# Kernel optimization log

Measured on AMD Instinct MI355X. Metric: run time of the kernel, lower is better.

Reference implementation:

```python
import jax, jax.numpy as jnp
import numpy as np

N = 100000   # nodes
E = 1600000  # edges
D = 128      # feature dim (layers all 128)
G = 512      # graphs in batch
C = 10       # num_classes
EPS = 1e-5   # batchnorm eps


def setup_inputs() -> dict:
    key = jax.random.key(0)
    ks = jax.random.split(key, 16)
    s = 1.0 / np.sqrt(D)
    return {
        "x": jax.random.normal(ks[0], (N, D), jnp.float32),
        "edge_index": jax.random.randint(ks[1], (2, E), 0, N),
        "batch": jnp.sort(jax.random.randint(ks[2], (N,), 0, G)),
        "w1": jax.random.normal(ks[3], (D, D), jnp.float32) * s,
        "b1": jnp.zeros((D,), jnp.float32),
        "w2": jax.random.normal(ks[4], (D, D), jnp.float32) * s,
        "b2": jnp.zeros((D,), jnp.float32),
        "w3": jax.random.normal(ks[5], (D, D), jnp.float32) * s,
        "b3": jnp.zeros((D,), jnp.float32),
        "g1": jnp.ones((D,), jnp.float32),
        "be1": jnp.zeros((D,), jnp.float32),
        "g2": jnp.ones((D,), jnp.float32),
        "be2": jnp.zeros((D,), jnp.float32),
        "fc_w": jax.random.normal(ks[6], (D, C), jnp.float32) * s,
        "fc_b": jnp.zeros((C,), jnp.float32),
    }


def _gcn(x, src, dst, norm, W, b):
    # transform -> gather -> normalize -> scatter-add (PyG GCNConv)
    h = x @ W
    out = jax.ops.segment_sum(h[src] * norm[:, None], dst, num_segments=x.shape[0])
    return out + b


def _bn(x, g, b):
    # training-mode BatchNorm1d: batch mean / biased variance
    mu = jnp.mean(x, axis=0)
    var = jnp.mean((x - mu) ** 2, axis=0)
    return (x - mu) * jax.lax.rsqrt(var + EPS) * g + b


def reference(x, edge_index, batch, w1, b1, w2, b2, w3, b3, g1, be1, g2, be2, fc_w, fc_b):
    n = x.shape[0]
    loop = jnp.arange(n)
    src = jnp.concatenate([edge_index[0], loop])  # add self-loops
    dst = jnp.concatenate([edge_index[1], loop])
    deg = jax.ops.segment_sum(jnp.ones_like(src, x.dtype), dst, num_segments=n)
    dinv = jax.lax.rsqrt(jnp.maximum(deg, 1.0))  # deg >= 1 due to self-loops
    norm = dinv[src] * dinv[dst]  # symmetric normalization per edge

    h = jax.nn.relu(_gcn(x, src, dst, norm, w1, b1))        # conv1 + relu (bn1 unused, per source)
    h = jax.nn.relu(_gcn(h, src, dst, norm, w2, b2))        # conv2 + relu
    h = jax.nn.relu(_bn(h, g1, be1))                        # bn + relu
    h = jax.nn.relu(_gcn(h, src, dst, norm, w3, b3))        # conv3 + relu
    h = jax.nn.relu(_bn(h, g2, be2))                        # bn + relu

    cnt = jax.ops.segment_sum(jnp.ones((n,), h.dtype), batch, num_segments=G)
    pooled = jax.ops.segment_sum(h, batch, num_segments=G) / jnp.maximum(cnt, 1.0)[:, None]
    logits = pooled @ fc_w + fc_b
    return jax.nn.log_softmax(logits, axis=1)
```

## Files before the change

### kernel.cpp

```cpp
#include <hip/hip_runtime.h>
#include <hip/hip_bf16.h>
#include <math.h>

#define D 128
#define G_GRAPHS 512
#define C_CLASSES 10
#define BN_EPS 1e-5f
#define NBUCK_MAX 512
#define EDGE_CHUNK 4096
#define EPT 16

typedef unsigned short u16;
typedef unsigned int u32;
typedef unsigned short ushort4_t __attribute__((ext_vector_type(4)));
typedef unsigned short ushort8_t __attribute__((ext_vector_type(8)));
typedef __bf16 bf16x8 __attribute__((ext_vector_type(8)));
typedef float floatx4 __attribute__((ext_vector_type(4)));
union B8 { ushort8_t u; bf16x8 b; };

__device__ __forceinline__ float bf_lo(u32 v) { return __uint_as_float(v << 16); }
__device__ __forceinline__ float bf_hi(u32 v) { return __uint_as_float(v & 0xffff0000u); }
__device__ __forceinline__ u16 f2bf(float f) {
    union { float f; u32 u; } x; x.f = f;
    u32 r = x.u + 0x7fff + ((x.u >> 16) & 1);
    return (u16)(r >> 16);
}
__device__ __forceinline__ u32 pack2bf(float a, float b) {
    return (u32)f2bf(a) | ((u32)f2bf(b) << 16);
}


__global__ __launch_bounds__(256) void bucket_hist_kernel(
    const int* __restrict__ dst, int* __restrict__ bucketCnt, int E, int nbuck)
{
    __shared__ int h[NBUCK_MAX];
    int tid = threadIdx.x;
    for (int i = tid; i < NBUCK_MAX; i += 256) h[i] = 0;
    __syncthreads();
    for (int i = blockIdx.x * 256 + tid; i < E; i += gridDim.x * 256)
        atomicAdd(&h[dst[i] >> 8], 1);
    __syncthreads();
    for (int i = tid; i < nbuck; i += 256)
        if (h[i]) atomicAdd(&bucketCnt[i], h[i]);
}

__global__ void scan_buckets_kernel(
    const int* __restrict__ bucketCnt, int* __restrict__ bucketBase,
    int* __restrict__ bucketCursor, int* __restrict__ rowPtr, int nbuck, int N, int E)
{
    __shared__ int buf[2][512];
    int tid = threadIdx.x;
    int v = (tid < nbuck) ? bucketCnt[tid] : 0;
    buf[0][tid] = v;
    __syncthreads();
    int cur = 0;
    for (int off = 1; off < 512; off <<= 1) {
        buf[1 - cur][tid] = buf[cur][tid] + ((tid >= off) ? buf[cur][tid - off] : 0);
        cur ^= 1;
        __syncthreads();
    }
    if (tid < nbuck) {
        int b = buf[cur][tid] - v;
        bucketBase[tid] = b;
        bucketCursor[tid] = b;
    }
    if (tid == 0) { bucketBase[nbuck] = E; rowPtr[N] = E; }
}

__global__ __launch_bounds__(256) void scatter_pairs_kernel(
    const int* __restrict__ src, const int* __restrict__ dst,
    int* __restrict__ bucketCursor, u32* __restrict__ pairs, int E)
{
    __shared__ int h[NBUCK_MAX];
    __shared__ int base[NBUCK_MAX];
    int tid = threadIdx.x;
    int e0 = blockIdx.x * EDGE_CHUNK;
    for (int i = tid; i < NBUCK_MAX; i += 256) h[i] = 0;
    __syncthreads();
    int s[EPT], d[EPT], r[EPT];
#pragma unroll
    for (int j = 0; j < EPT; ++j) {
        int i = e0 + j * 256 + tid;
        if (i < E) {
            s[j] = src[i];
            d[j] = dst[i];
            r[j] = atomicAdd(&h[d[j] >> 8], 1);
        } else {
            d[j] = -1;
        }
    }
    __syncthreads();
    for (int i = tid; i < NBUCK_MAX; i += 256)
        if (h[i]) base[i] = atomicAdd(&bucketCursor[i], h[i]);
    __syncthreads();
#pragma unroll
    for (int j = 0; j < EPT; ++j) {
        if (d[j] >= 0) {
            int b = d[j] >> 8;
            pairs[base[b] + r[j]] = ((u32)s[j] << 8) | (u32)(d[j] & 255);
        }
    }
}

__global__ __launch_bounds__(256) void bucket_sort_kernel(
    const u32* __restrict__ pairs, const int* __restrict__ bucketBase,
    int* __restrict__ colIdx, int* __restrict__ rowPtr, float* __restrict__ dinv, int N)
{
    __shared__ int h[256];
    __shared__ int cur[256];
    __shared__ int sbuf[2][256];
    int tid = threadIdx.x;
    int b = blockIdx.x;
    int s = bucketBase[b], e = bucketBase[b + 1];
    h[tid] = 0;
    __syncthreads();
    for (int i = s + tid; i < e; i += 256)
        atomicAdd(&h[pairs[i] & 255], 1);
    __syncthreads();
    int cnt = h[tid];
    sbuf[0][tid] = cnt;
    __syncthreads();
    int c = 0;
    for (int off = 1; off < 256; off <<= 1) {
        sbuf[1 - c][tid] = sbuf[c][tid] + ((tid >= off) ? sbuf[c][tid - off] : 0);
        c ^= 1;
        __syncthreads();
    }
    int excl = sbuf[c][tid] - cnt;
    int v = b * 256 + tid;
    if (v < N) {
        rowPtr[v] = s + excl;
        dinv[v] = rsqrtf((float)(cnt + 1));
    }
    cur[tid] = s + excl;
    __syncthreads();
    for (int i = s + tid; i < e; i += 256) {
        u32 p = pairs[i];
        int pos = atomicAdd(&cur[p & 255], 1);
        colIdx[pos] = (int)(p >> 8);
    }
}

__global__ __launch_bounds__(256) void graph_bounds_kernel(
    const int* __restrict__ batch, int* __restrict__ gstart, int N)
{
    int i = blockIdx.x * 256 + threadIdx.x;
    if (i >= N) return;
    int b = batch[i];
    int prev = (i == 0) ? -1 : batch[i - 1];
    if (b != prev) {
        for (int g = prev + 1; g <= b; ++g) gstart[g] = i;
    }
    if (i == N - 1) {
        for (int g = b + 1; g <= G_GRAPHS; ++g) gstart[g] = N;
    }
}

__global__ __launch_bounds__(256) void wconv_kernel(
    const float4* __restrict__ w1, const float4* __restrict__ w2,
    const float4* __restrict__ w3, u16* __restrict__ wtAll)
{
    const float4* W = (blockIdx.x == 0) ? w1 : (blockIdx.x == 1) ? w2 : w3;
    u16* Wt = wtAll + (size_t)blockIdx.x * D * D;
    int tid = threadIdx.x;
#pragma unroll
    for (int i = 0; i < 16; ++i) {
        int idx = tid + i * 256;
        int k = idx >> 5, c4 = idx & 31;
        float4 v = W[idx];
        Wt[(4 * c4 + 0) * D + k] = f2bf(v.x);
        Wt[(4 * c4 + 1) * D + k] = f2bf(v.y);
        Wt[(4 * c4 + 2) * D + k] = f2bf(v.z);
        Wt[(4 * c4 + 3) * D + k] = f2bf(v.w);
    }
}

#define XS_STRIDE 136
#define GEMM_GRID 768

__device__ __forceinline__ void gemm_core_and_store(
    const u16* Xs, const u16* Ws, const float* __restrict__ dinv,
    u16* __restrict__ Y, int row0, int nrows, int tid)
{
    int wid = tid >> 6, lane = tid & 63;
    int m = lane & 15, quad = lane >> 4;
    int xrow = wid * 16 + m;

    floatx4 acc[8] = {};
#pragma unroll
    for (int ks = 0; ks < 4; ++ks) {
        int kk = ks * 32 + quad * 8;
        B8 a;
        a.u = *(const ushort8_t*)&Xs[xrow * XS_STRIDE + kk];
#pragma unroll
        for (int t = 0; t < 8; ++t) {
            B8 b;
            b.u = *(const ushort8_t*)&Ws[(t * 16 + m) * XS_STRIDE + kk];
            acc[t] = __builtin_amdgcn_mfma_f32_16x16x32_bf16(b.b, a.b, acc[t], 0, 0, 0);
        }
    }
    int grow = row0 + xrow;
    if (grow < nrows) {
        float du = dinv[grow];
#pragma unroll
        for (int t = 0; t < 8; ++t) {
            ushort4_t o;
            o.x = f2bf(acc[t][0] * du); o.y = f2bf(acc[t][1] * du);
            o.z = f2bf(acc[t][2] * du); o.w = f2bf(acc[t][3] * du);
            *(ushort4_t*)&Y[(size_t)grow * D + t * 16 + quad * 4] = o;
        }
    }
}

__device__ __forceinline__ void stage_w(const u16* __restrict__ Wt, u16* Ws, int tid) {
    const ushort8_t* Wv = (const ushort8_t*)Wt;
#pragma unroll
    for (int i = 0; i < 8; ++i) {
        int idx = tid + i * 256;
        int n = idx >> 4, c8 = idx & 15;
        *(ushort8_t*)&Ws[n * XS_STRIDE + c8 * 8] = Wv[idx];
    }
}

__global__ __launch_bounds__(256) void gemm_mfma_f32in_kernel(
    const float4* __restrict__ X, const u16* __restrict__ Wt,
    const float* __restrict__ dinv, u16* __restrict__ Y, int nrows, int ntiles)
{
    __shared__ __align__(16) u16 Xs[64 * XS_STRIDE];
    __shared__ __align__(16) u16 Ws[128 * XS_STRIDE];
    int tid = threadIdx.x;
    stage_w(Wt, Ws, tid);
    for (int t = blockIdx.x; t < ntiles; t += gridDim.x) {
        int row0 = t * 64;
        __syncthreads();
#pragma unroll
        for (int i = 0; i < 8; ++i) {
            int idx = tid + i * 256;
            int r = idx >> 5, c4 = idx & 31;
            int gr = row0 + r;
            float4 v = make_float4(0.f, 0.f, 0.f, 0.f);
            if (gr < nrows) v = X[(size_t)gr * 32 + c4];
            ushort4_t o;
            o.x = f2bf(v.x); o.y = f2bf(v.y); o.z = f2bf(v.z); o.w = f2bf(v.w);
            *(ushort4_t*)&Xs[r * XS_STRIDE + c4 * 4] = o;
        }
        __syncthreads();
        gemm_core_and_store(Xs, Ws, dinv, Y, row0, nrows, tid);
    }
}

__global__ __launch_bounds__(256) void gemm_mfma_bf16in_kernel(
    const uint4* __restrict__ X, const u16* __restrict__ Wt,
    const float* __restrict__ gsum, const float* __restrict__ gsq,
    const float* __restrict__ gamma, const float* __restrict__ beta, float invN,
    const float* __restrict__ dinv, u16* __restrict__ Y, int nrows, int ntiles)
{
    __shared__ __align__(16) u16 Xs[64 * XS_STRIDE];
    __shared__ __align__(16) u16 Ws[128 * XS_STRIDE];
    __shared__ float scs[D], shs[D];
    int tid = threadIdx.x;
    bool fuse = (gsum != nullptr);
    stage_w(Wt, Ws, tid);
    if (fuse && tid < D) {
        float mu = gsum[tid] * invN;
        float var = gsq[tid] * invN - mu * mu;
        float sc = gamma[tid] * rsqrtf(var + BN_EPS);
        scs[tid] = sc;
        shs[tid] = beta[tid] - mu * sc;
    }
    for (int t = blockIdx.x; t < ntiles; t += gridDim.x) {
        int row0 = t * 64;
        __syncthreads();
#pragma unroll
        for (int i = 0; i < 4; ++i) {
            int idx = tid + i * 256;
            int r = idx >> 4, c8 = idx & 15;
            int gr = row0 + r;
            uint4 v = make_uint4(0, 0, 0, 0);
            if (gr < nrows) v = X[(size_t)gr * 16 + c8];
            if (fuse) {
                int k = c8 * 8;
                v.x = pack2bf(fmaxf(bf_lo(v.x) * scs[k]     + shs[k],     0.f),
                              fmaxf(bf_hi(v.x) * scs[k + 1] + shs[k + 1], 0.f));
                v.y = pack2bf(fmaxf(bf_lo(v.y) * scs[k + 2] + shs[k + 2], 0.f),
                              fmaxf(bf_hi(v.y) * scs[k + 3] + shs[k + 3], 0.f));
                v.z = pack2bf(fmaxf(bf_lo(v.z) * scs[k + 4] + shs[k + 4], 0.f),
                              fmaxf(bf_hi(v.z) * scs[k + 5] + shs[k + 5], 0.f));
                v.w = pack2bf(fmaxf(bf_lo(v.w) * scs[k + 6] + shs[k + 6], 0.f),
                              fmaxf(bf_hi(v.w) * scs[k + 7] + shs[k + 7], 0.f));
            }
            *(uint4*)&Xs[r * XS_STRIDE + c8 * 8] = v;
        }
        __syncthreads();
        gemm_core_and_store(Xs, Ws, dinv, Y, row0, nrows, tid);
    }
}

#define ACCV(tw)                                       \
    acc0 += bf_lo((tw).x); acc1 += bf_hi((tw).x);      \
    acc2 += bf_lo((tw).y); acc3 += bf_hi((tw).y);      \
    acc4 += bf_lo((tw).z); acc5 += bf_hi((tw).z);      \
    acc6 += bf_lo((tw).w); acc7 += bf_hi((tw).w);

__global__ __launch_bounds__(256) void aggregate_kernel(
    const uint4* __restrict__ T, const int* __restrict__ colIdx,
    const int* __restrict__ rowPtr, const float* __restrict__ dinv,
    const float* __restrict__ bias, u32* __restrict__ outH, int n)
{
    int tid = threadIdx.x;
    int fg = tid & 15;
    int grp = tid >> 4;
    int row = blockIdx.x * 16 + grp;
    if (row >= n) return;

    const char* baseT = (const char*)T + fg * 16;

    uint4 sv = *(const uint4*)(baseT + ((size_t)(u32)row << 8));
    float acc0 = bf_lo(sv.x), acc1 = bf_hi(sv.x);
    float acc2 = bf_lo(sv.y), acc3 = bf_hi(sv.y);
    float acc4 = bf_lo(sv.z), acc5 = bf_hi(sv.z);
    float acc6 = bf_lo(sv.w), acc7 = bf_hi(sv.w);

    int s = rowPtr[row], e = rowPtr[row + 1];
    int j = s;
    for (; j + 4 <= e; j += 4) {
        int u0 = colIdx[j];
        int u1 = colIdx[j + 1];
        int u2 = colIdx[j + 2];
        int u3 = colIdx[j + 3];
        uint4 t0 = *(const uint4*)(baseT + ((size_t)(u32)u0 << 8));
        uint4 t1 = *(const uint4*)(baseT + ((size_t)(u32)u1 << 8));
        uint4 t2 = *(const uint4*)(baseT + ((size_t)(u32)u2 << 8));
        uint4 t3 = *(const uint4*)(baseT + ((size_t)(u32)u3 << 8));
        ACCV(t0); ACCV(t1); ACCV(t2); ACCV(t3);
    }
    for (; j < e; ++j) {
        int u = colIdx[j];
        uint4 t = *(const uint4*)(baseT + ((size_t)(u32)u << 8));
        ACCV(t);
    }

    float dr = dinv[row];
    const float2* bp = (const float2*)bias;
    float2 b0 = bp[fg * 4 + 0];
    float2 b1 = bp[fg * 4 + 1];
    float2 b2 = bp[fg * 4 + 2];
    float2 b3 = bp[fg * 4 + 3];
    uint4 o;
    o.x = pack2bf(fmaxf(dr * acc0 + b0.x, 0.f), fmaxf(dr * acc1 + b0.y, 0.f));
    o.y = pack2bf(fmaxf(dr * acc2 + b1.x, 0.f), fmaxf(dr * acc3 + b1.y, 0.f));
    o.z = pack2bf(fmaxf(dr * acc4 + b2.x, 0.f), fmaxf(dr * acc5 + b2.y, 0.f));
    o.w = pack2bf(fmaxf(dr * acc6 + b3.x, 0.f), fmaxf(dr * acc7 + b3.y, 0.f));
    *(uint4*)&outH[(size_t)row * 64 + fg * 4] = o;
}

__global__ __launch_bounds__(256) void bn_stats_kernel(
    const u32* __restrict__ H, int n, float* __restrict__ gsum, float* __restrict__ gsq)
{
    int tid = threadIdx.x;
    int c = tid & 63, rr = tid >> 6;
    float sA = 0.f, sA2 = 0.f, sB = 0.f, sB2 = 0.f;
    for (int row = blockIdx.x * 4 + rr; row < n; row += gridDim.x * 4) {
        u32 v = H[(size_t)row * 64 + c];
        float a = bf_lo(v), b = bf_hi(v);
        sA += a; sA2 += a * a; sB += b; sB2 += b * b;
    }
    __shared__ float shA[256], shA2[256], shB[256], shB2[256];
    shA[tid] = sA; shA2[tid] = sA2; shB[tid] = sB; shB2[tid] = sB2;
    __syncthreads();
    if (tid < 64) {
        float tA = shA[tid] + shA[tid + 64] + shA[tid + 128] + shA[tid + 192];
        float tA2 = shA2[tid] + shA2[tid + 64] + shA2[tid + 128] + shA2[tid + 192];
        float tB = shB[tid] + shB[tid + 64] + shB[tid + 128] + shB[tid + 192];
        float tB2 = shB2[tid] + shB2[tid + 64] + shB2[tid + 128] + shB2[tid + 192];
        atomicAdd(&gsum[2 * c], tA);
        atomicAdd(&gsq[2 * c], tA2);
        atomicAdd(&gsum[2 * c + 1], tB);
        atomicAdd(&gsq[2 * c + 1], tB2);
    }
}

__global__ __launch_bounds__(256) void pool_classify_kernel(
    const u32* __restrict__ H, const float* __restrict__ gsum, const float* __restrict__ gsq,
    const float* __restrict__ gamma, const float* __restrict__ beta, float invN,
    const int* __restrict__ gstart, const float* __restrict__ fcw,
    const float* __restrict__ fcb, float* __restrict__ out)
{
    int g = blockIdx.x;
    int tid = threadIdx.x;
    int c = tid & 63, q = tid >> 6;
    float muA = gsum[2 * c] * invN, muB = gsum[2 * c + 1] * invN;
    float vA = gsq[2 * c] * invN - muA * muA, vB = gsq[2 * c + 1] * invN - muB * muB;
    float scA = gamma[2 * c] * rsqrtf(vA + BN_EPS), scB = gamma[2 * c + 1] * rsqrtf(vB + BN_EPS);
    float shA = beta[2 * c] - muA * scA, shB = beta[2 * c + 1] - muB * scB;

    int s = gstart[g], cnt = gstart[g + 1] - s;
    float aA = 0.f, aB = 0.f;
    for (int i = q; i < cnt; i += 4) {
        u32 v = H[(size_t)(s + i) * 64 + c];
        aA += fmaxf(bf_lo(v) * scA + shA, 0.f);
        aB += fmaxf(bf_hi(v) * scB + shB, 0.f);
    }
    __shared__ float sA[256], sB[256];
    __shared__ float prow[D];
    __shared__ float lg[C_CLASSES];
    sA[tid] = aA; sB[tid] = aB;
    __syncthreads();
    if (tid < 64) {
        float tA = sA[tid] + sA[tid + 64] + sA[tid + 128] + sA[tid + 192];
        float tB = sB[tid] + sB[tid + 64] + sB[tid + 128] + sB[tid + 192];
        float inv = 1.f / (float)(cnt > 1 ? cnt : 1);
        prow[2 * tid] = tA * inv;
        prow[2 * tid + 1] = tB * inv;
    }
    __syncthreads();
    if (tid < C_CLASSES) {
        float sum = fcb[tid];
        for (int d = 0; d < D; ++d) sum += prow[d] * fcw[d * C_CLASSES + tid];
        lg[tid] = sum;
    }
    __syncthreads();
    if (tid == 0) {
        float mx = -1e30f;
        for (int k = 0; k < C_CLASSES; ++k) mx = fmaxf(mx, lg[k]);
        float se = 0.f;
        for (int k = 0; k < C_CLASSES; ++k) se += expf(lg[k] - mx);
        float lse = mx + logf(se);
        for (int k = 0; k < C_CLASSES; ++k) out[(size_t)g * C_CLASSES + k] = lg[k] - lse;
    }
}

extern "C" void kernel_launch(void* const* d_in, const int* in_sizes, int n_in,
                              void* d_out, int out_size, void* d_ws, size_t ws_size,
                              hipStream_t stream) {
    const float* x   = (const float*)d_in[0];
    const int* ei    = (const int*)d_in[1];
    const int* batch = (const int*)d_in[2];
    const float* w1  = (const float*)d_in[3];
    const float* b1  = (const float*)d_in[4];
    const float* w2  = (const float*)d_in[5];
    const float* b2  = (const float*)d_in[6];
    const float* w3  = (const float*)d_in[7];
    const float* b3  = (const float*)d_in[8];
    const float* g1  = (const float*)d_in[9];
    const float* be1 = (const float*)d_in[10];
    const float* g2  = (const float*)d_in[11];
    const float* be2 = (const float*)d_in[12];
    const float* fcw = (const float*)d_in[13];
    const float* fcb = (const float*)d_in[14];

    const int N = in_sizes[0] / D;
    const int E = in_sizes[1] / 2;
    const int* src = ei;
    const int* dst = ei + E;
    const int nbuck = (N + 255) >> 8;
    const float invN = 1.f / (float)N;

    char* p = (char*)d_ws;
    auto alloc = [&](size_t bytes) -> void* {
        void* r = (void*)p;
        p += (bytes + 255) & ~(size_t)255;
        return r;
    };
    int*   bucketCnt    = (int*)alloc(NBUCK_MAX * 4);
    float* statsacc     = (float*)alloc(4 * D * 4);
    float* gsum1 = statsacc, *gsq1 = statsacc + D, *gsum2 = statsacc + 2 * D, *gsq2 = statsacc + 3 * D;
    float* dinv     = (float*)alloc((size_t)N * 4);
    int*   rowPtr   = (int*)alloc((size_t)(N + 1) * 4);
    int*   colIdx   = (int*)alloc((size_t)E * 4);
    u32*   pairs    = (u32*)alloc((size_t)E * 4);
    int*   bucketBase   = (int*)alloc((NBUCK_MAX + 1) * 4);
    int*   bucketCursor = (int*)alloc(NBUCK_MAX * 4);
    int*   gstart  = (int*)alloc((G_GRAPHS + 1) * 4);
    u16*   wtAll   = (u16*)alloc((size_t)3 * D * D * 2);
    u16*   tmp     = (u16*)alloc((size_t)N * D * 2);
    u16*   hbuf    = (u16*)alloc((size_t)N * D * 2);

    hipMemsetAsync(bucketCnt, 0, NBUCK_MAX * 4 + 4 * D * 4, stream);

    bucket_hist_kernel<<<512, 256, 0, stream>>>(dst, bucketCnt, E, nbuck);
    scan_buckets_kernel<<<1, 512, 0, stream>>>(bucketCnt, bucketBase, bucketCursor, rowPtr, nbuck, N, E);
    scatter_pairs_kernel<<<(E + EDGE_CHUNK - 1) / EDGE_CHUNK, 256, 0, stream>>>(src, dst, bucketCursor, pairs, E);
    bucket_sort_kernel<<<nbuck, 256, 0, stream>>>(pairs, bucketBase, colIdx, rowPtr, dinv, N);
    graph_bounds_kernel<<<(N + 255) / 256, 256, 0, stream>>>(batch, gstart, N);
    wconv_kernel<<<3, 256, 0, stream>>>((const float4*)w1, (const float4*)w2, (const float4*)w3, wtAll);

    const int NT = (N + 63) / 64;
    const int GB = NT < GEMM_GRID ? NT : GEMM_GRID;
    const int AB = (N + 15) / 16;

    gemm_mfma_f32in_kernel<<<GB, 256, 0, stream>>>((const float4*)x, wtAll, dinv, tmp, N, NT);
    aggregate_kernel<<<AB, 256, 0, stream>>>((const uint4*)tmp, colIdx, rowPtr, dinv, b1, (u32*)hbuf, N);
    gemm_mfma_bf16in_kernel<<<GB, 256, 0, stream>>>((const uint4*)hbuf, wtAll + D * D,
        nullptr, nullptr, nullptr, nullptr, 0.f, dinv, tmp, N, NT);
    aggregate_kernel<<<AB, 256, 0, stream>>>((const uint4*)tmp, colIdx, rowPtr, dinv, b2, (u32*)hbuf, N);
    bn_stats_kernel<<<256, 256, 0, stream>>>((const u32*)hbuf, N, gsum1, gsq1);
    gemm_mfma_bf16in_kernel<<<GB, 256, 0, stream>>>((const uint4*)hbuf, wtAll + 2 * D * D,
        gsum1, gsq1, g1, be1, invN, dinv, tmp, N, NT);
    aggregate_kernel<<<AB, 256, 0, stream>>>((const uint4*)tmp, colIdx, rowPtr, dinv, b3, (u32*)hbuf, N);
    bn_stats_kernel<<<256, 256, 0, stream>>>((const u32*)hbuf, N, gsum2, gsq2);
    pool_classify_kernel<<<G_GRAPHS, 256, 0, stream>>>((const u32*)hbuf, gsum2, gsq2, g2, be2, invN,
        gstart, fcw, fcb, (float*)d_out);
}
```

Baseline: 507.8 us.

## Software-pipeline neighbor gathers in aggregation using a zero-row sentinel

The aggregation kernel now gathers neighbor rows in batches of eight with double buffering: the next batch is loaded while the current one is accumulated. Out-of-range slots point at an extra zeroed row appended to the transformed-feature buffer, so the loop has no scalar tail. The goal is more memory-level parallelism on the latency-bound random gather. The change also sets a min-blocks-per-CU launch bound of 4 and raises the BN stats grid to 1024 blocks. In exchange it pads work for low-degree rows, reads colIdx past a row's end (those values are masked out, but the reads can run beyond the colIdx allocation), and uses more registers.

Result: slower. 922.0 us (+81.6%).

```diff
diff --git a/kernel.cpp b/kernel.cpp
--- a/kernel.cpp
+++ b/kernel.cpp
@@ -158,11 +158,15 @@
 
 __global__ __launch_bounds__(256) void wconv_kernel(
     const float4* __restrict__ w1, const float4* __restrict__ w2,
-    const float4* __restrict__ w3, u16* __restrict__ wtAll)
-{
+    const float4* __restrict__ w3, u16* __restrict__ wtAll, u32* __restrict__ tzero)
+{
+    int tid = threadIdx.x;
+    if (blockIdx.x == 3) {
+        if (tid < 64) tzero[tid] = 0;
+        return;
+    }
     const float4* W = (blockIdx.x == 0) ? w1 : (blockIdx.x == 1) ? w2 : w3;
     u16* Wt = wtAll + (size_t)blockIdx.x * D * D;
-    int tid = threadIdx.x;
 #pragma unroll
     for (int i = 0; i < 16; ++i) {
         int idx = tid + i * 256;
@@ -296,16 +300,16 @@
     }
 }
 
-#define ACCV(tw)                                       \
-    acc0 += bf_lo((tw).x); acc1 += bf_hi((tw).x);      \
-    acc2 += bf_lo((tw).y); acc3 += bf_hi((tw).y);      \
-    acc4 += bf_lo((tw).z); acc5 += bf_hi((tw).z);      \
-    acc6 += bf_lo((tw).w); acc7 += bf_hi((tw).w);
-
-__global__ __launch_bounds__(256) void aggregate_kernel(
+#define ACC8U(t)                                           \
+    acc0 += bf_lo((t).x); acc1 += bf_hi((t).x);            \
+    acc2 += bf_lo((t).y); acc3 += bf_hi((t).y);            \
+    acc4 += bf_lo((t).z); acc5 += bf_hi((t).z);            \
+    acc6 += bf_lo((t).w); acc7 += bf_hi((t).w);
+
+__global__ __launch_bounds__(256, 4) void aggregate_kernel(
     const uint4* __restrict__ T, const int* __restrict__ colIdx,
     const int* __restrict__ rowPtr, const float* __restrict__ dinv,
-    const float* __restrict__ bias, u32* __restrict__ outH, int n)
+    const float* __restrict__ bias, u32* __restrict__ outH, int n, u32 zoff)
 {
     int tid = threadIdx.x;
     int fg = tid & 15;
@@ -322,35 +326,88 @@
     float acc6 = bf_lo(sv.w), acc7 = bf_hi(sv.w);
 
     int s = rowPtr[row], e = rowPtr[row + 1];
-    int j = s;
-    for (; j + 4 <= e; j += 4) {
-        int u0 = colIdx[j];
-        int u1 = colIdx[j + 1];
-        int u2 = colIdx[j + 2];
-        int u3 = colIdx[j + 3];
-        uint4 t0 = *(const uint4*)(baseT + ((size_t)(u32)u0 << 8));
-        uint4 t1 = *(const uint4*)(baseT + ((size_t)(u32)u1 << 8));
-        uint4 t2 = *(const uint4*)(baseT + ((size_t)(u32)u2 << 8));
-        uint4 t3 = *(const uint4*)(baseT + ((size_t)(u32)u3 << 8));
-        ACCV(t0); ACCV(t1); ACCV(t2); ACCV(t3);
-    }
-    for (; j < e; ++j) {
-        int u = colIdx[j];
-        uint4 t = *(const uint4*)(baseT + ((size_t)(u32)u << 8));
-        ACCV(t);
+    int len = e - s;
+    const int* ci = colIdx + s;
+
+    if (len > 0) {
+        int nsb = (len + 15) >> 4;
+        u32 oA[8], oB[8];
+#pragma unroll
+        for (int k = 0; k < 8; ++k) {
+            int u = ci[k];
+            oA[k] = (k < len) ? ((u32)u << 8) : zoff;
+        }
+        uint4 a0 = *(const uint4*)(baseT + oA[0]);
+        uint4 a1 = *(const uint4*)(baseT + oA[1]);
+        uint4 a2 = *(const uint4*)(baseT + oA[2]);
+        uint4 a3 = *(const uint4*)(baseT + oA[3]);
+        uint4 a4 = *(const uint4*)(baseT + oA[4]);
+        uint4 a5 = *(const uint4*)(baseT + oA[5]);
+        uint4 a6 = *(const uint4*)(baseT + oA[6]);
+        uint4 a7 = *(const uint4*)(baseT + oA[7]);
+#pragma unroll
+        for (int k = 0; k < 8; ++k) {
+            int j = 8 + k;
+            int u = ci[j];
+            oB[k] = (j < len) ? ((u32)u << 8) : zoff;
+        }
+        int sb = 0;
+#pragma unroll 1
+        for (;;) {
+            uint4 b0 = *(const uint4*)(baseT + oB[0]);
+            uint4 b1 = *(const uint4*)(baseT + oB[1]);
+            uint4 b2 = *(const uint4*)(baseT + oB[2]);
+            uint4 b3 = *(const uint4*)(baseT + oB[3]);
+            uint4 b4 = *(const uint4*)(baseT + oB[4]);
+            uint4 b5 = *(const uint4*)(baseT + oB[5]);
+            uint4 b6 = *(const uint4*)(baseT + oB[6]);
+            uint4 b7 = *(const uint4*)(baseT + oB[7]);
+            int jb = sb * 16 + 16;
+            ++sb;
+            bool more = (sb < nsb);
+#pragma unroll
+            for (int k = 0; k < 8; ++k) {
+                int j = jb + k;
+                int u = ci[j];
+                oA[k] = (j < len) ? ((u32)u << 8) : zoff;
+            }
+            ACC8U(a0); ACC8U(a1); ACC8U(a2); ACC8U(a3);
+            ACC8U(a4); ACC8U(a5); ACC8U(a6); ACC8U(a7);
+            if (!more) {
+                ACC8U(b0); ACC8U(b1); ACC8U(b2); ACC8U(b3);
+                ACC8U(b4); ACC8U(b5); ACC8U(b6); ACC8U(b7);
+                break;
+            }
+            a0 = *(const uint4*)(baseT + oA[0]);
+            a1 = *(const uint4*)(baseT + oA[1]);
+            a2 = *(const uint4*)(baseT + oA[2]);
+            a3 = *(const uint4*)(baseT + oA[3]);
+            a4 = *(const uint4*)(baseT + oA[4]);
+            a5 = *(const uint4*)(baseT + oA[5]);
+            a6 = *(const uint4*)(baseT + oA[6]);
+            a7 = *(const uint4*)(baseT + oA[7]);
+#pragma unroll
+            for (int k = 0; k < 8; ++k) {
+                int j = jb + 8 + k;
+                int u = ci[j];
+                oB[k] = (j < len) ? ((u32)u << 8) : zoff;
+            }
+            ACC8U(b0); ACC8U(b1); ACC8U(b2); ACC8U(b3);
+            ACC8U(b4); ACC8U(b5); ACC8U(b6); ACC8U(b7);
+        }
     }
 
     float dr = dinv[row];
     const float2* bp = (const float2*)bias;
-    float2 b0 = bp[fg * 4 + 0];
-    float2 b1 = bp[fg * 4 + 1];
-    float2 b2 = bp[fg * 4 + 2];
-    float2 b3 = bp[fg * 4 + 3];
+    float2 bq0 = bp[fg * 4 + 0];
+    float2 bq1 = bp[fg * 4 + 1];
+    float2 bq2 = bp[fg * 4 + 2];
+    float2 bq3 = bp[fg * 4 + 3];
     uint4 o;
-    o.x = pack2bf(fmaxf(dr * acc0 + b0.x, 0.f), fmaxf(dr * acc1 + b0.y, 0.f));
-    o.y = pack2bf(fmaxf(dr * acc2 + b1.x, 0.f), fmaxf(dr * acc3 + b1.y, 0.f));
-    o.z = pack2bf(fmaxf(dr * acc4 + b2.x, 0.f), fmaxf(dr * acc5 + b2.y, 0.f));
-    o.w = pack2bf(fmaxf(dr * acc6 + b3.x, 0.f), fmaxf(dr * acc7 + b3.y, 0.f));
+    o.x = pack2bf(fmaxf(dr * acc0 + bq0.x, 0.f), fmaxf(dr * acc1 + bq0.y, 0.f));
+    o.y = pack2bf(fmaxf(dr * acc2 + bq1.x, 0.f), fmaxf(dr * acc3 + bq1.y, 0.f));
+    o.z = pack2bf(fmaxf(dr * acc4 + bq2.x, 0.f), fmaxf(dr * acc5 + bq2.y, 0.f));
+    o.w = pack2bf(fmaxf(dr * acc6 + bq3.x, 0.f), fmaxf(dr * acc7 + bq3.y, 0.f));
     *(uint4*)&outH[(size_t)row * 64 + fg * 4] = o;
 }
 
@@ -473,7 +530,7 @@
     int*   bucketCursor = (int*)alloc(NBUCK_MAX * 4);
     int*   gstart  = (int*)alloc((G_GRAPHS + 1) * 4);
     u16*   wtAll   = (u16*)alloc((size_t)3 * D * D * 2);
-    u16*   tmp     = (u16*)alloc((size_t)N * D * 2);
+    u16*   tmp     = (u16*)alloc((size_t)(N + 1) * D * 2);
     u16*   hbuf    = (u16*)alloc((size_t)N * D * 2);
 
     hipMemsetAsync(bucketCnt, 0, NBUCK_MAX * 4 + 4 * D * 4, stream);
@@ -483,22 +540,24 @@
     scatter_pairs_kernel<<<(E + EDGE_CHUNK - 1) / EDGE_CHUNK, 256, 0, stream>>>(src, dst, bucketCursor, pairs, E);
     bucket_sort_kernel<<<nbuck, 256, 0, stream>>>(pairs, bucketBase, colIdx, rowPtr, dinv, N);
     graph_bounds_kernel<<<(N + 255) / 256, 256, 0, stream>>>(batch, gstart, N);
-    wconv_kernel<<<3, 256, 0, stream>>>((const float4*)w1, (const float4*)w2, (const float4*)w3, wtAll);
+    wconv_kernel<<<4, 256, 0, stream>>>((const float4*)w1, (const float4*)w2, (const float4*)w3,
+                                        wtAll, (u32*)(tmp + (size_t)N * D));
 
     const int NT = (N + 63) / 64;
     const int GB = NT < GEMM_GRID ? NT : GEMM_GRID;
     const int AB = (N + 15) / 16;
+    const u32 ZOFF = (u32)N << 8;
 
     gemm_mfma_f32in_kernel<<<GB, 256, 0, stream>>>((const float4*)x, wtAll, dinv, tmp, N, NT);
-    aggregate_kernel<<<AB, 256, 0, stream>>>((const uint4*)tmp, colIdx, rowPtr, dinv, b1, (u32*)hbuf, N);
+    aggregate_kernel<<<AB, 256, 0, stream>>>((const uint4*)tmp, colIdx, rowPtr, dinv, b1, (u32*)hbuf, N, ZOFF);
     gemm_mfma_bf16in_kernel<<<GB, 256, 0, stream>>>((const uint4*)hbuf, wtAll + D * D,
         nullptr, nullptr, nullptr, nullptr, 0.f, dinv, tmp, N, NT);
-    aggregate_kernel<<<AB, 256, 0, stream>>>((const uint4*)tmp, colIdx, rowPtr, dinv, b2, (u32*)hbuf, N);
-    bn_stats_kernel<<<256, 256, 0, stream>>>((const u32*)hbuf, N, gsum1, gsq1);
+    aggregate_kernel<<<AB, 256, 0, stream>>>((const uint4*)tmp, colIdx, rowPtr, dinv, b2, (u32*)hbuf, N, ZOFF);
+    bn_stats_kernel<<<1024, 256, 0, stream>>>((const u32*)hbuf, N, gsum1, gsq1);
     gemm_mfma_bf16in_kernel<<<GB, 256, 0, stream>>>((const uint4*)hbuf, wtAll + 2 * D * D,
         gsum1, gsq1, g1, be1, invN, dinv, tmp, N, NT);
-    aggregate_kernel<<<AB, 256, 0, stream>>>((const uint4*)tmp, colIdx, rowPtr, dinv, b3, (u32*)hbuf, N);
-    bn_stats_kernel<<<256, 256, 0, stream>>>((const u32*)hbuf, N, gsum2, gsq2);
+    aggregate_kernel<<<AB, 256, 0, stream>>>((const uint4*)tmp, colIdx, rowPtr, dinv, b3, (u32*)hbuf, N, ZOFF);
+    bn_stats_kernel<<<1024, 256, 0, stream>>>((const u32*)hbuf, N, gsum2, gsq2);
     pool_classify_kernel<<<G_GRAPHS, 256, 0, stream>>>((const u32*)hbuf, gsum2, gsq2, g2, be2, invN,
         gstart, fcw, fcb, (float*)d_out);
 }
```
